# Optimization experiments

Hardware: AMD Instinct MI355X
Metric: run time of the kernel (lower is better)

The kernel has to match this reference:

```python
import jax, jax.numpy as jnp
import numpy as np

IN_F = 4096
OUT_F = 11008
GROUP = 128
BATCH = 32
Q_OUT = OUT_F // 2          # two int4 values packed per byte along out dim
N_GROUPS = IN_F // GROUP    # 32 groups


def setup_inputs() -> dict:
    key = jax.random.key(0)
    k1, k2, k3, k4, k5 = jax.random.split(key, 5)
    inp = jax.random.normal(k1, (BATCH, 1, IN_F), dtype=jnp.float32)
    qweight = jax.random.randint(k2, (IN_F, Q_OUT), 0, 256, dtype=jnp.int32)   # packed bytes
    scales = jax.random.uniform(k3, (N_GROUPS, OUT_F), dtype=jnp.float32) * 0.01
    qzeros = jax.random.randint(k4, (N_GROUPS, Q_OUT), 0, 256, dtype=jnp.int32)  # packed bytes
    bias = jax.random.normal(k5, (OUT_F,), dtype=jnp.float32)
    return {"input": inp, "qweight": qweight, "scales": scales, "qzeros": qzeros, "bias": bias}


def _unpack_int4(packed, n_out):
    # packed: [rows, n_out//2] bytes; low nibble -> even out col, high nibble -> odd out col
    low = packed & 0xF
    high = (packed >> 4) & 0xF
    return jnp.stack([low, high], axis=-1).reshape(packed.shape[0], n_out)


def reference(input, qweight, scales, qzeros, bias):
    # GPTQ-style grouped dequant: w[k, n] = (q[k, n] - zero[g(k), n]) * scale[g(k), n]
    q = _unpack_int4(qweight, OUT_F).astype(jnp.float32)   # [K, N]
    z = _unpack_int4(qzeros, OUT_F).astype(jnp.float32)    # [G, N]
    gidx = jnp.arange(IN_F) // GROUP                       # [K] group index per input channel
    w = (q - z[gidx]) * scales[gidx]                       # [K, N] dequantized weight
    # decode GEMV/GEMM: [B, 1, K] x [K, N] -> [B, 1, N], plus bias (mm_bias_int4 path)
    return jnp.einsum('bsk,kn->bsn', input, w) + bias
```

## Files before the change

### kernel.cpp

```cpp
#include <hip/hip_runtime.h>
#include <cstdint>

#define IN_F 4096
#define OUT_F 11008
#define Q_OUT 5504
#define GROUP 128
#define BATCH 32

#define KBS 4
#define GPB 8
#define NCH 16
#define BN 64
#define BST 18

typedef int   i32x4 __attribute__((ext_vector_type(4)));
typedef float f32x4 __attribute__((ext_vector_type(4)));

__global__ __launch_bounds__(256)
void prep_kernel(const float* __restrict__ x,
                 const float* __restrict__ bias,
                 uint4* __restrict__ xq,
                 int*   __restrict__ Sx,
                 float* __restrict__ delta,
                 float* __restrict__ out)
{
    const int t = threadIdx.x;
    if (blockIdx.x >= 32) {
        const int base = (blockIdx.x - 32) * 4096 + t * 16;
        #pragma unroll
        for (int i = 0; i < 4; ++i)
            *reinterpret_cast<float4*>(out + base + i * 4) =
                *reinterpret_cast<const float4*>(bias + ((base + i * 4) % OUT_F));
        return;
    }
    const int m = blockIdx.x;
    const float* xr = x + (size_t)m * IN_F + t * 16;
    float4 v[4];
    #pragma unroll
    for (int i = 0; i < 4; ++i) v[i] = reinterpret_cast<const float4*>(xr)[i];

    float lm = 0.f;
    #pragma unroll
    for (int i = 0; i < 4; ++i) {
        lm = fmaxf(lm, fmaxf(fmaxf(fabsf(v[i].x), fabsf(v[i].y)),
                             fmaxf(fabsf(v[i].z), fabsf(v[i].w))));
    }
    #pragma unroll
    for (int d = 32; d; d >>= 1) lm = fmaxf(lm, __shfl_xor(lm, d));
    __shared__ float wred[4];
    if ((t & 63) == 0) wred[t >> 6] = lm;
    __syncthreads();
    const float mx  = fmaxf(fmaxf(wred[0], wred[1]), fmaxf(wred[2], wred[3]));
    const float inv = mx > 0.f ? 127.0f / mx : 0.f;

    int q[16];
    #pragma unroll
    for (int i = 0; i < 4; ++i) {
        q[i * 4 + 0] = __float2int_rn(v[i].x * inv);
        q[i * 4 + 1] = __float2int_rn(v[i].y * inv);
        q[i * 4 + 2] = __float2int_rn(v[i].z * inv);
        q[i * 4 + 3] = __float2int_rn(v[i].w * inv);
    }
    uint4 w;
    uint* wp = reinterpret_cast<uint*>(&w);
    #pragma unroll
    for (int i = 0; i < 4; ++i)
        wp[i] = (q[i*4] & 255) | ((q[i*4+1] & 255) << 8) |
                ((q[i*4+2] & 255) << 16) | ((q[i*4+3] & 255) << 24);
    xq[(t >> 2) * 128 + (m >> 4) * 64 + (t & 3) * 16 + (m & 15)] = w;

    int psum = 0;
    #pragma unroll
    for (int i = 0; i < 16; ++i) psum += q[i];
    #pragma unroll
    for (int d = 4; d; d >>= 1) psum += __shfl_down(psum, d, 8);
    if ((t & 7) == 0) Sx[(t >> 3) * 32 + m] = psum;
    if (t == 0) delta[m] = mx * (1.0f / 127.0f);
}

__global__ __launch_bounds__(256, 3)
void int4_gemm_i8(const uint4* __restrict__ xq,
                  const int*   __restrict__ qw,
                  const float* __restrict__ scales,
                  const int*   __restrict__ qz,
                  const int*   __restrict__ Sx,
                  const float* __restrict__ delta,
                  float*       __restrict__ out)
{
    const int tid  = threadIdx.x;
    const int lane = tid & 63;
    const int wid  = tid >> 6;
    const int nb   = blockIdx.x;
    const int kb   = blockIdx.y;
    const int g0   = kb * GPB;
    const int k0b  = g0 * GROUP;

    __shared__ int b_lds[2][32 * BST];

    const int cl  = lane & 15;
    const int kg  = lane >> 4;
    const int n   = nb * BN + wid * 16 + cl;
    const int w   = wid * 8 + (cl >> 1);
    const int shn = (cl & 1) * 4;

    int   zv[GPB];
    float sv[GPB];
    #pragma unroll
    for (int g = 0; g < GPB; ++g) {
        sv[g] = scales[(size_t)(g0 + g) * OUT_F + n];
        zv[g] = (qz[(size_t)(g0 + g) * Q_OUT + (n >> 1)] >> shn) & 15;
    }

    const int a16 = tid & 15;
    const int rk  = tid >> 4;

    uint2 d[2][4];
    uint4 A[2][2];
    i32x4 acc_i[2] = {};
    f32x4 accf[2]  = {};
    int4  sx0v = {}, sx1v = {};

    auto LOADB = [&](int c, int set) {
        const int kr = k0b + c * 64 + 4 * rk;
        #pragma unroll
        for (int i = 0; i < 4; ++i)
            d[set][i] = *reinterpret_cast<const uint2*>(
                qw + (size_t)(kr + i) * Q_OUT + nb * 32 + 2 * a16);
    };
    auto LOADA = [&](int c, int set) {
        const uint4* ab = xq + (size_t)kb * (NCH * 128) + c * 128;
        A[set][0] = ab[lane];
        A[set][1] = ab[64 + lane];
    };
    auto WLDS = [&](int buf, int set) {
        #pragma unroll
        for (int j = 0; j < 2; ++j) {
            uint b0 = (j ? d[set][0].y : d[set][0].x) & 255u;
            uint b1 = (j ? d[set][1].y : d[set][1].x) & 255u;
            uint b2 = (j ? d[set][2].y : d[set][2].x) & 255u;
            uint b3 = (j ? d[set][3].y : d[set][3].x) & 255u;
            b_lds[buf][(2 * a16 + j) * BST + rk] =
                (int)(b0 | (b1 << 8) | (b2 << 16) | (b3 << 24));
        }
    };

    LOADB(0, 0);
    LOADA(0, 0);
    LOADB(1, 1);
    LOADA(1, 1);
    WLDS(0, 0);
    asm volatile("s_waitcnt lgkmcnt(0)" ::: "memory");
    __builtin_amdgcn_s_barrier();
    asm volatile("" ::: "memory");

    #pragma unroll
    for (int c = 0; c < NCH; ++c) {
        const int cur = c & 1;
        const int gl  = c >> 1;
        if (c + 2 < NCH) LOADB(c + 2, cur);
        if ((c & 1) == 0) {
            sx0v = *reinterpret_cast<const int4*>(Sx + (g0 + gl) * 32 + kg * 4);
            sx1v = *reinterpret_cast<const int4*>(Sx + (g0 + gl) * 32 + 16 + kg * 4);
        }

        const int* bp = &b_lds[cur][w * BST + 4 * kg];
        int4 qp = *reinterpret_cast<const int4*>(bp);
        i32x4 bv;
        bv[0] = (int)(((uint)qp.x >> shn) & 0x0F0F0F0Fu);
        bv[1] = (int)(((uint)qp.y >> shn) & 0x0F0F0F0Fu);
        bv[2] = (int)(((uint)qp.z >> shn) & 0x0F0F0F0Fu);
        bv[3] = (int)(((uint)qp.w >> shn) & 0x0F0F0F0Fu);

        acc_i[0] = __builtin_amdgcn_mfma_i32_16x16x64_i8(
            __builtin_bit_cast(i32x4, A[cur][0]), bv, acc_i[0], 0, 0, 0);
        acc_i[1] = __builtin_amdgcn_mfma_i32_16x16x64_i8(
            __builtin_bit_cast(i32x4, A[cur][1]), bv, acc_i[1], 0, 0, 0);

        if (c + 2 < NCH) LOADA(c + 2, cur);

        if (c & 1) {
            const int   zz = zv[gl];
            const float ss = sv[gl];
            int sxa[8] = { sx0v.x, sx0v.y, sx0v.z, sx0v.w,
                           sx1v.x, sx1v.y, sx1v.z, sx1v.w };
            #pragma unroll
            for (int f = 0; f < 2; ++f)
                #pragma unroll
                for (int r = 0; r < 4; ++r) {
                    int tt = acc_i[f][r] - zz * sxa[f * 4 + r];
                    accf[f][r] = fmaf(ss, (float)tt, accf[f][r]);
                }
            acc_i[0] = i32x4{0, 0, 0, 0};
            acc_i[1] = i32x4{0, 0, 0, 0};
        }

        if (c + 1 < NCH) {
            WLDS(cur ^ 1, cur ^ 1);
            asm volatile("s_waitcnt lgkmcnt(0)" ::: "memory");
            __builtin_amdgcn_s_barrier();
            asm volatile("" ::: "memory");
        }
    }

    float4 dl0 = *reinterpret_cast<const float4*>(delta + kg * 4);
    float4 dl1 = *reinterpret_cast<const float4*>(delta + 16 + kg * 4);
    const float dla[8] = { dl0.x, dl0.y, dl0.z, dl0.w, dl1.x, dl1.y, dl1.z, dl1.w };
    #pragma unroll
    for (int f = 0; f < 2; ++f)
        #pragma unroll
        for (int r = 0; r < 4; ++r) {
            const int m = f * 16 + kg * 4 + r;
            unsafeAtomicAdd(out + (size_t)m * OUT_F + n, dla[f * 4 + r] * accf[f][r]);
        }
}

extern "C" void kernel_launch(void* const* d_in, const int* in_sizes, int n_in,
                              void* d_out, int out_size, void* d_ws, size_t ws_size,
                              hipStream_t stream)
{
    const float* inp    = (const float*)d_in[0];
    const int*   qw     = (const int*)d_in[1];
    const float* scales = (const float*)d_in[2];
    const int*   qz     = (const int*)d_in[3];
    const float* bias   = (const float*)d_in[4];
    float*       out    = (float*)d_out;

    uint4* xq    = (uint4*)d_ws;
    int*   Sx    = (int*)((char*)d_ws + 131072);
    float* delta = (float*)((char*)d_ws + 131072 + 4096);

    prep_kernel<<<118, 256, 0, stream>>>(inp, bias, xq, Sx, delta, out);

    int4_gemm_i8<<<dim3(OUT_F / BN, KBS), 256, 0, stream>>>(
        xq, qw, scales, qz, Sx, delta, out);
}
```

Baseline: 30.39 us.

## Widen N tile to 128 with two MFMA column fragments per wave and deeper K split

Each wave now covers 32 output columns using two 16-wide MFMA fragments that reuse the same activation operands. Weight rows are fetched with 16-byte loads and repacked into a larger LDS tile. The K dimension is split across 16 blocks instead of 4, giving more blocks and shorter per-block loops to hide memory latency. The cost is four times as many atomic adds into the output, plus unaligned scalar LDS reads because of the odd row stride.

```diff
diff --git a/kernel.cpp b/kernel.cpp
--- a/kernel.cpp
+++ b/kernel.cpp
@@ -7,11 +7,11 @@
 #define GROUP 128
 #define BATCH 32
 
-#define KBS 4
-#define GPB 8
-#define NCH 16
-#define BN 64
-#define BST 18
+#define KBS 16
+#define GPB 2
+#define NCH 4
+#define BN 128
+#define BST 21
 
 typedef int   i32x4 __attribute__((ext_vector_type(4)));
 typedef float f32x4 __attribute__((ext_vector_type(4)));
@@ -93,54 +93,56 @@
     const int nb   = blockIdx.x;
     const int kb   = blockIdx.y;
     const int g0   = kb * GPB;
-    const int k0b  = g0 * GROUP;
-
-    __shared__ int b_lds[2][32 * BST];
+    const int k0b  = kb * (NCH * 64);
+
+    __shared__ int b_lds[2][64 * BST];
 
     const int cl  = lane & 15;
     const int kg  = lane >> 4;
-    const int n   = nb * BN + wid * 16 + cl;
-    const int w   = wid * 8 + (cl >> 1);
+    const int n   = nb * BN + wid * 32 + (0) * 16 + cl;
     const int shn = (cl & 1) * 4;
 
-    int   zv[GPB];
-    float sv[GPB];
-    #pragma unroll
-    for (int g = 0; g < GPB; ++g) {
-        sv[g] = scales[(size_t)(g0 + g) * OUT_F + n];
-        zv[g] = (qz[(size_t)(g0 + g) * Q_OUT + (n >> 1)] >> shn) & 15;
-    }
-
-    const int a16 = tid & 15;
-    const int rk  = tid >> 4;
-
-    uint2 d[2][4];
+    float sv[GPB][2];
+    int   zv[GPB][2];
+    #pragma unroll
+    for (int g = 0; g < GPB; ++g)
+        #pragma unroll
+        for (int nf = 0; nf < 2; ++nf) {
+            const int nn = n + nf * 16;
+            sv[g][nf] = scales[(size_t)(g0 + g) * OUT_F + nn];
+            zv[g][nf] = (qz[(size_t)(g0 + g) * Q_OUT + (nn >> 1)] >> shn) & 15;
+        }
+
+    const int c16 = lane & 15;
+    const int qr  = lane >> 4;
+
+    uint4 d[2][4];
     uint4 A[2][2];
-    i32x4 acc_i[2] = {};
-    f32x4 accf[2]  = {};
+    i32x4 acc_i[2][2] = {};
+    f32x4 accf[2][2]  = {};
     int4  sx0v = {}, sx1v = {};
 
     auto LOADB = [&](int c, int set) {
-        const int kr = k0b + c * 64 + 4 * rk;
-        #pragma unroll
-        for (int i = 0; i < 4; ++i)
-            d[set][i] = *reinterpret_cast<const uint2*>(
-                qw + (size_t)(kr + i) * Q_OUT + nb * 32 + 2 * a16);
+        const int kr = k0b + c * 64 + 16 * wid + 4 * qr;
+        #pragma unroll
+        for (int r = 0; r < 4; ++r)
+            d[set][r] = *reinterpret_cast<const uint4*>(
+                qw + (size_t)(kr + r) * Q_OUT + nb * 64 + 4 * c16);
     };
     auto LOADA = [&](int c, int set) {
-        const uint4* ab = xq + (size_t)kb * (NCH * 128) + c * 128;
+        const uint4* ab = xq + (size_t)(kb * NCH + c) * 128;
         A[set][0] = ab[lane];
         A[set][1] = ab[64 + lane];
     };
     auto WLDS = [&](int buf, int set) {
-        #pragma unroll
-        for (int j = 0; j < 2; ++j) {
-            uint b0 = (j ? d[set][0].y : d[set][0].x) & 255u;
-            uint b1 = (j ? d[set][1].y : d[set][1].x) & 255u;
-            uint b2 = (j ? d[set][2].y : d[set][2].x) & 255u;
-            uint b3 = (j ? d[set][3].y : d[set][3].x) & 255u;
-            b_lds[buf][(2 * a16 + j) * BST + rk] =
-                (int)(b0 | (b1 << 8) | (b2 << 16) | (b3 << 24));
+        const int kd = 4 * wid + qr;
+        #pragma unroll
+        for (int j = 0; j < 4; ++j) {
+            uint pw = (((uint*)&d[set][0])[j])        |
+                      ((((uint*)&d[set][1])[j]) << 8)  |
+                      ((((uint*)&d[set][2])[j]) << 16) |
+                      ((((uint*)&d[set][3])[j]) << 24);
+            b_lds[buf][(4 * c16 + j) * BST + kd] = (int)pw;
         }
     };
 
@@ -163,35 +165,40 @@
             sx1v = *reinterpret_cast<const int4*>(Sx + (g0 + gl) * 32 + 16 + kg * 4);
         }
 
-        const int* bp = &b_lds[cur][w * BST + 4 * kg];
-        int4 qp = *reinterpret_cast<const int4*>(bp);
-        i32x4 bv;
-        bv[0] = (int)(((uint)qp.x >> shn) & 0x0F0F0F0Fu);
-        bv[1] = (int)(((uint)qp.y >> shn) & 0x0F0F0F0Fu);
-        bv[2] = (int)(((uint)qp.z >> shn) & 0x0F0F0F0Fu);
-        bv[3] = (int)(((uint)qp.w >> shn) & 0x0F0F0F0Fu);
-
-        acc_i[0] = __builtin_amdgcn_mfma_i32_16x16x64_i8(
-            __builtin_bit_cast(i32x4, A[cur][0]), bv, acc_i[0], 0, 0, 0);
-        acc_i[1] = __builtin_amdgcn_mfma_i32_16x16x64_i8(
-            __builtin_bit_cast(i32x4, A[cur][1]), bv, acc_i[1], 0, 0, 0);
+        #pragma unroll
+        for (int nf = 0; nf < 2; ++nf) {
+            const int nw = wid * 16 + nf * 8 + (cl >> 1);
+            const int* bp = &b_lds[cur][nw * BST + 4 * kg];
+            i32x4 bv;
+            bv[0] = (int)(((uint)bp[0] >> shn) & 0x0F0F0F0Fu);
+            bv[1] = (int)(((uint)bp[1] >> shn) & 0x0F0F0F0Fu);
+            bv[2] = (int)(((uint)bp[2] >> shn) & 0x0F0F0F0Fu);
+            bv[3] = (int)(((uint)bp[3] >> shn) & 0x0F0F0F0Fu);
+            acc_i[0][nf] = __builtin_amdgcn_mfma_i32_16x16x64_i8(
+                __builtin_bit_cast(i32x4, A[cur][0]), bv, acc_i[0][nf], 0, 0, 0);
+            acc_i[1][nf] = __builtin_amdgcn_mfma_i32_16x16x64_i8(
+                __builtin_bit_cast(i32x4, A[cur][1]), bv, acc_i[1][nf], 0, 0, 0);
+        }
 
         if (c + 2 < NCH) LOADA(c + 2, cur);
 
         if (c & 1) {
-            const int   zz = zv[gl];
-            const float ss = sv[gl];
             int sxa[8] = { sx0v.x, sx0v.y, sx0v.z, sx0v.w,
                            sx1v.x, sx1v.y, sx1v.z, sx1v.w };
             #pragma unroll
             for (int f = 0; f < 2; ++f)
                 #pragma unroll
-                for (int r = 0; r < 4; ++r) {
-                    int tt = acc_i[f][r] - zz * sxa[f * 4 + r];
-                    accf[f][r] = fmaf(ss, (float)tt, accf[f][r]);
-                }
-            acc_i[0] = i32x4{0, 0, 0, 0};
-            acc_i[1] = i32x4{0, 0, 0, 0};
+                for (int nf = 0; nf < 2; ++nf)
+                    #pragma unroll
+                    for (int r = 0; r < 4; ++r) {
+                        int tt = acc_i[f][nf][r] - zv[gl][nf] * sxa[f * 4 + r];
+                        accf[f][nf][r] = fmaf(sv[gl][nf], (float)tt, accf[f][nf][r]);
+                    }
+            #pragma unroll
+            for (int f = 0; f < 2; ++f)
+                #pragma unroll
+                for (int nf = 0; nf < 2; ++nf)
+                    acc_i[f][nf] = i32x4{0, 0, 0, 0};
         }
 
         if (c + 1 < NCH) {
@@ -208,10 +215,13 @@
     #pragma unroll
     for (int f = 0; f < 2; ++f)
         #pragma unroll
-        for (int r = 0; r < 4; ++r) {
-            const int m = f * 16 + kg * 4 + r;
-            unsafeAtomicAdd(out + (size_t)m * OUT_F + n, dla[f * 4 + r] * accf[f][r]);
-        }
+        for (int nf = 0; nf < 2; ++nf)
+            #pragma unroll
+            for (int r = 0; r < 4; ++r) {
+                const int m = f * 16 + kg * 4 + r;
+                unsafeAtomicAdd(out + (size_t)m * OUT_F + n + nf * 16,
+                                dla[f * 4 + r] * accf[f][nf][r]);
+            }
 }
 
 extern "C" void kernel_launch(void* const* d_in, const int* in_sizes, int n_in,
```

Result: slower. 35.19 us (+15.8%).

## Use per-wave LDS staging without block barriers and double K-split

Applied to the files above, without the earlier changes.

Each wave now loads and stages only its own 16 output columns of packed weights into a private LDS region, so the block-wide barriers between chunks are replaced by a plain lgkmcnt wait. Nibble unpacking moves from the LDS read side to the LDS write side, and the K split is raised from 4 to 8 blocks with fewer groups per block, with launch bounds asking for 4 blocks per CU. This is meant to remove barrier stalls and increase parallelism, at the cost of more atomic adds to the output and narrower per-wave global loads.

```diff
diff --git a/kernel.cpp b/kernel.cpp
--- a/kernel.cpp
+++ b/kernel.cpp
@@ -7,9 +7,9 @@
 #define GROUP 128
 #define BATCH 32
 
-#define KBS 4
-#define GPB 8
-#define NCH 16
+#define KBS 8
+#define GPB 4
+#define NCH 8
 #define BN 64
 #define BST 18
 
@@ -78,7 +78,7 @@
     if (t == 0) delta[m] = mx * (1.0f / 127.0f);
 }
 
-__global__ __launch_bounds__(256, 3)
+__global__ __launch_bounds__(256, 4)
 void int4_gemm_i8(const uint4* __restrict__ xq,
                   const int*   __restrict__ qw,
                   const float* __restrict__ scales,
@@ -95,12 +95,12 @@
     const int g0   = kb * GPB;
     const int k0b  = g0 * GROUP;
 
-    __shared__ int b_lds[2][32 * BST];
+    __shared__ int b_lds[4][2][16 * BST];
+    int (*bl)[16 * BST] = b_lds[wid];
 
     const int cl  = lane & 15;
     const int kg  = lane >> 4;
     const int n   = nb * BN + wid * 16 + cl;
-    const int w   = wid * 8 + (cl >> 1);
     const int shn = (cl & 1) * 4;
 
     int   zv[GPB];
@@ -111,8 +111,8 @@
         zv[g] = (qz[(size_t)(g0 + g) * Q_OUT + (n >> 1)] >> shn) & 15;
     }
 
-    const int a16 = tid & 15;
-    const int rk  = tid >> 4;
+    const int rq = lane & 15;
+    const int ip = lane >> 4;
 
     uint2 d[2][4];
     uint4 A[2][2];
@@ -121,14 +121,14 @@
     int4  sx0v = {}, sx1v = {};
 
     auto LOADB = [&](int c, int set) {
-        const int kr = k0b + c * 64 + 4 * rk;
+        const int kr = k0b + c * 64 + 4 * rq;
         #pragma unroll
         for (int i = 0; i < 4; ++i)
             d[set][i] = *reinterpret_cast<const uint2*>(
-                qw + (size_t)(kr + i) * Q_OUT + nb * 32 + 2 * a16);
+                qw + (size_t)(kr + i) * Q_OUT + nb * 32 + wid * 8 + 2 * ip);
     };
     auto LOADA = [&](int c, int set) {
-        const uint4* ab = xq + (size_t)kb * (NCH * 128) + c * 128;
+        const uint4* ab = xq + (size_t)kb * 1024 + c * 128;
         A[set][0] = ab[lane];
         A[set][1] = ab[64 + lane];
     };
@@ -139,8 +139,10 @@
             uint b1 = (j ? d[set][1].y : d[set][1].x) & 255u;
             uint b2 = (j ? d[set][2].y : d[set][2].x) & 255u;
             uint b3 = (j ? d[set][3].y : d[set][3].x) & 255u;
-            b_lds[buf][(2 * a16 + j) * BST + rk] =
-                (int)(b0 | (b1 << 8) | (b2 << 16) | (b3 << 24));
+            uint p  = b0 | (b1 << 8) | (b2 << 16) | (b3 << 24);
+            const int nl = 4 * ip + 2 * j;
+            bl[buf][(nl + 0) * BST + rq] = (int)(p & 0x0F0F0F0Fu);
+            bl[buf][(nl + 1) * BST + rq] = (int)((p >> 4) & 0x0F0F0F0Fu);
         }
     };
 
@@ -149,9 +151,6 @@
     LOADB(1, 1);
     LOADA(1, 1);
     WLDS(0, 0);
-    asm volatile("s_waitcnt lgkmcnt(0)" ::: "memory");
-    __builtin_amdgcn_s_barrier();
-    asm volatile("" ::: "memory");
 
     #pragma unroll
     for (int c = 0; c < NCH; ++c) {
@@ -163,13 +162,12 @@
             sx1v = *reinterpret_cast<const int4*>(Sx + (g0 + gl) * 32 + 16 + kg * 4);
         }
 
-        const int* bp = &b_lds[cur][w * BST + 4 * kg];
-        int4 qp = *reinterpret_cast<const int4*>(bp);
-        i32x4 bv;
-        bv[0] = (int)(((uint)qp.x >> shn) & 0x0F0F0F0Fu);
-        bv[1] = (int)(((uint)qp.y >> shn) & 0x0F0F0F0Fu);
-        bv[2] = (int)(((uint)qp.z >> shn) & 0x0F0F0F0Fu);
-        bv[3] = (int)(((uint)qp.w >> shn) & 0x0F0F0F0Fu);
+        asm volatile("s_waitcnt lgkmcnt(0)" ::: "memory");
+
+        const int* bp = &bl[cur][cl * BST + 4 * kg];
+        int2 qa = *reinterpret_cast<const int2*>(bp);
+        int2 qb = *reinterpret_cast<const int2*>(bp + 2);
+        i32x4 bv; bv[0] = qa.x; bv[1] = qa.y; bv[2] = qb.x; bv[3] = qb.y;
 
         acc_i[0] = __builtin_amdgcn_mfma_i32_16x16x64_i8(
             __builtin_bit_cast(i32x4, A[cur][0]), bv, acc_i[0], 0, 0, 0);
@@ -194,12 +192,7 @@
             acc_i[1] = i32x4{0, 0, 0, 0};
         }
 
-        if (c + 1 < NCH) {
-            WLDS(cur ^ 1, cur ^ 1);
-            asm volatile("s_waitcnt lgkmcnt(0)" ::: "memory");
-            __builtin_amdgcn_s_barrier();
-            asm volatile("" ::: "memory");
-        }
+        if (c + 1 < NCH) WLDS(cur ^ 1, cur ^ 1);
     }
 
     float4 dl0 = *reinterpret_cast<const float4*>(delta + kg * 4);
```

After: 39.91 us. 31.3% more time.
